# Kernel optimization log

Hardware: AMD Instinct MI355X
Metric: run time of the kernel (lower is better)

Reference implementation:

```python
import jax, jax.numpy as jnp
import numpy as np

L, B, T, N, C, H, K, M = 2, 4, 8, 2048, 2, 64, 3, 32
DIN0, DIN1, DOUT = C + H, 2 * H, 4 * H


def setup_inputs() -> dict:
    key = jax.random.key(0)
    ks = jax.random.split(key, 24)
    s = 0.05
    p = lambda k, shape: jax.random.normal(k, shape, jnp.float32) * s
    return {
        # support matrices, roughly row-normalized random graph
        "G": jax.random.uniform(ks[0], (K, N, N), jnp.float32) * (2.0 / N),
        "x_seq": jax.random.normal(ks[1], (B, T, N, C), jnp.float32),
        "init_h": jnp.zeros((L, B, N, H), jnp.float32),
        "init_c": jnp.zeros((L, B, N, H), jnp.float32),
        "x_meta": jax.random.normal(ks[2], (B, T, M), jnp.float32),
        # layer 0 meta-learner params (dim_in = C+H)
        "lw1_0": p(ks[3], (M, 64)), "lb1_0": p(ks[4], (64,)),
        "lw2_0": p(ks[5], (64, K * DIN0 * DOUT)), "lb2_0": p(ks[6], (K * DIN0 * DOUT,)),
        "bw1_0": p(ks[7], (M, 64)), "bb1_0": p(ks[8], (64,)),
        "bw2_0": p(ks[9], (64, DOUT)), "bb2_0": p(ks[10], (DOUT,)),
        # layer 1 meta-learner params (dim_in = 2H)
        "lw1_1": p(ks[11], (M, 64)), "lb1_1": p(ks[12], (64,)),
        "lw2_1": p(ks[13], (64, K * DIN1 * DOUT)), "lb2_1": p(ks[14], (K * DIN1 * DOUT,)),
        "bw1_1": p(ks[15], (M, 64)), "bb1_1": p(ks[16], (64,)),
        "bw2_1": p(ks[17], (64, DOUT)), "bb2_1": p(ks[18], (DOUT,)),
    }


def _meta_gcn(G, x, meta, lw1, lb1, lw2, lb2, bw1, bb1, bw2, bb2):
    # x: [B, N, din] -> out: [B, N, 4H]
    Bb, Nn, din = x.shape
    # K-hop supports, concatenated along feature dim (k-major, matches torch.cat)
    sup = jnp.einsum('kij,bjd->bikd', G, x).reshape(Bb, Nn, K * din)
    W = (jax.nn.relu(meta @ lw1 + lb1) @ lw2 + lb2).reshape(Bb, K * din, DOUT)
    b = (jax.nn.relu(meta @ bw1 + bb1) @ bw2 + bb2)[:, None, :]
    return jnp.einsum('bnd,bdo->bno', sup, W) + b


def _run_layer(G, xs_t, meta_t, h0, c0, params):
    # xs_t: [T, B, N, din_x], meta_t: [T, B, M]
    def step(carry, inp):
        h, c = carry
        x_t, m_t = inp
        conv = _meta_gcn(G, jnp.concatenate([x_t, h], axis=-1), m_t, *params)
        gi, gf, go, gg = jnp.split(conv, 4, axis=-1)
        c_t = jax.nn.sigmoid(gf) * c + jax.nn.sigmoid(gi) * jnp.tanh(gg)
        h_t = jax.nn.sigmoid(go) * jnp.tanh(c_t)
        return (h_t, c_t), h_t
    (hT, cT), hs = jax.lax.scan(step, (h0, c0), (xs_t, meta_t))
    return hT, cT, hs


def reference(G, x_seq, init_h, init_c, x_meta,
              lw1_0, lb1_0, lw2_0, lb2_0, bw1_0, bb1_0, bw2_0, bb2_0,
              lw1_1, lb1_1, lw2_1, lb2_1, bw1_1, bb1_1, bw2_1, bb2_1):
    xs = jnp.transpose(x_seq, (1, 0, 2, 3))      # [T, B, N, C]
    ms = jnp.transpose(x_meta, (1, 0, 2))        # [T, B, M]
    p0 = (lw1_0, lb1_0, lw2_0, lb2_0, bw1_0, bb1_0, bw2_0, bb2_0)
    p1 = (lw1_1, lb1_1, lw2_1, lb2_1, bw1_1, bb1_1, bw2_1, bb2_1)
    h0T, c0T, hs0 = _run_layer(G, xs, ms, init_h[0], init_c[0], p0)
    h1T, c1T, _ = _run_layer(G, hs0, ms, init_h[1], init_c[1], p1)
    # [2, L, B, N, H]: [final h per layer; final c per layer]
    return jnp.stack([jnp.stack([h0T, h1T]), jnp.stack([c0T, c1T])])
```

## Files before the change

### kernel.cpp

```cpp
#include <hip/hip_runtime.h>
#include <hip/hip_bf16.h>
#include <cstdint>


typedef __hip_bfloat16 bf16;
typedef __attribute__((ext_vector_type(8))) short bf16x8;
typedef __attribute__((ext_vector_type(4))) short s16x4;
typedef __attribute__((ext_vector_type(4)))  float f32x4;
typedef __attribute__((ext_vector_type(16))) float f32x16;
typedef __attribute__((ext_vector_type(4)))  int   i32x4;
typedef __attribute__((ext_vector_type(16))) int   i32x16;
typedef __attribute__((ext_vector_type(2)))  long  l64x2;

__device__ __forceinline__ short f2bf(float f) {
    unsigned u = __builtin_bit_cast(unsigned, f);
    return (short)((u + 0x7fffu + ((u >> 16) & 1u)) >> 16);
}

#define GLD_LDS(gaddr, laddr)                                                  \
    __builtin_amdgcn_global_load_lds(                                          \
        (const __attribute__((address_space(1))) void*)(gaddr),                \
        (__attribute__((address_space(3))) void*)(laddr), 16, 0, 0)

#define OFF_GSW    0u
#define OFF_GI8    25165824u
#define OFF_HFA0   37748736u
#define OFF_HFA1   38273024u
#define OFF_HFB0   38797312u
#define OFF_HFB1   39321600u
#define OFF_XS0T   39845888u
#define OFF_HS0F   40370176u
#define OFF_S0X    48758784u
#define OFF_W0SW   74711040u
#define OFF_W1SW   79429632u
#define OFF_BIAS0  85721088u
#define OFF_BIAS1  85753856u
#define OFF_C0     85786624u
#define OFF_C1     87883776u
#define WS_NEEDED  89980928u

__global__ __launch_bounds__(256) void prep_kernel(
    const float* __restrict__ G, const float* __restrict__ x_seq,
    const float* __restrict__ init_h, const float* __restrict__ init_c,
    bf16* __restrict__ Gsw, l64x2* __restrict__ Gi8,
    l64x2* __restrict__ hfA0, l64x2* __restrict__ hfA1,
    bf16* __restrict__ Xs0T, float* __restrict__ c0, float* __restrict__ c1)
{
    const int T_GSB = 1572864;
    const int T_GI8 = 786432;
    const int T_HF  = 65536;
    const int T_XS  = 262144;
    const int T_C   = 1048576;
    const int TOTAL = T_GSB + T_GI8 + T_HF + T_XS + T_C;
    int stride = gridDim.x * 256;
    for (int idx = blockIdx.x*256 + threadIdx.x; idx < TOTAL; idx += stride) {
        int i0 = idx;
        if (i0 < T_GSB) {
            int lane = i0 & 63, jc = (i0 >> 6) & 127, it32 = (i0 >> 13) & 63, k = i0 >> 19;
            int row = it32*32 + (lane & 31);
            int col = jc*16 + (lane >> 5)*8;
            const float* gp = G + ((size_t)(k*2048 + row))*2048 + col;
            f32x4 v0 = *(const f32x4*)gp, v1 = *(const f32x4*)(gp + 4);
            bf16x8 o;
            #pragma unroll
            for (int e = 0; e < 4; e++) { o[e] = f2bf(v0[e]); o[e+4] = f2bf(v1[e]); }
            *(bf16x8*)((short*)Gsw + (size_t)i0*8) = o;
            continue;
        }
        i0 -= T_GSB;
        if (i0 < T_GI8) {
            int lane = i0 & 63, jcp = (i0 >> 6) & 63, it = (i0 >> 12) & 63, k = i0 >> 18;
            int row = it*32 + (lane & 31);
            l64x2 pr;
            #pragma unroll
            for (int jh = 0; jh < 2; jh++) {
                int col = (2*jcp + jh)*16 + (lane >> 5)*8;
                const float* gp = G + ((size_t)(k*2048 + row))*2048 + col;
                f32x4 v0 = *(const f32x4*)gp, v1 = *(const f32x4*)(gp + 4);
                long r = 0;
                #pragma unroll
                for (int e = 0; e < 4; e++) {
                    int q0 = __float2int_rn(v0[e] * 130048.0f);
                    int q1 = __float2int_rn(v1[e] * 130048.0f);
                    q0 = q0 < 0 ? 0 : (q0 > 127 ? 127 : q0);
                    q1 = q1 < 0 ? 0 : (q1 > 127 ? 127 : q1);
                    r |= ((long)(unsigned char)(char)q0) << (8*e);
                    r |= ((long)(unsigned char)(char)q1) << (8*(e+4));
                }
                pr[jh] = r;
            }
            Gi8[i0] = pr;
            continue;
        }
        i0 -= T_GI8;
        if (i0 < T_HF) {
            int lane = i0 & 63, dc = (i0 >> 6) & 1, jcp = (i0 >> 7) & 63;
            int b = (i0 >> 13) & 3, L = i0 >> 15;
            int d = dc*32 + (lane & 31);
            l64x2 pr;
            #pragma unroll
            for (int jh = 0; jh < 2; jh++) {
                int j0 = (2*jcp + jh)*16 + (lane >> 5)*8;
                long r = 0;
                #pragma unroll
                for (int e = 0; e < 8; e++) {
                    float hv = init_h[((size_t)(L*4 + b)*2048 + j0 + e)*64 + d];
                    int q = __float2int_rn(hv * 127.0f);
                    q = q < -127 ? -127 : (q > 127 ? 127 : q);
                    r |= ((long)(unsigned char)(char)q) << (8*e);
                }
                pr[jh] = r;
            }
            l64x2* dst = (L == 0) ? hfA0 : hfA1;
            dst[i0 & 32767] = pr;
            continue;
        }
        i0 -= T_HF;
        if (i0 < T_XS) {
            int n = i0 >> 11, j = i0 & 2047;
            float v = 0.f;
            if (n < 64) {
                int t = n >> 3, rm = n & 7, b = rm >> 1, cc = rm & 1;
                v = x_seq[(((size_t)b*8 + t)*2048 + j)*2 + cc];
            }
            Xs0T[i0] = __float2bfloat16(v);
            continue;
        }
        i0 -= T_XS;
        if (i0 < 524288) { c0[i0] = init_c[i0]; continue; }
        i0 -= 524288;
        c1[i0] = init_c[524288 + i0];
    }
}

__global__ __launch_bounds__(256) void metaw_kernel(
    const float* __restrict__ x_meta,
    const float* __restrict__ lw1_0, const float* __restrict__ lb1_0,
    const float* __restrict__ lw2_0, const float* __restrict__ lb2_0,
    const float* __restrict__ bw1_0, const float* __restrict__ bb1_0,
    const float* __restrict__ bw2_0, const float* __restrict__ bb2_0,
    const float* __restrict__ lw1_1, const float* __restrict__ lb1_1,
    const float* __restrict__ lw2_1, const float* __restrict__ lb2_1,
    const float* __restrict__ bw1_1, const float* __restrict__ bb1_1,
    const float* __restrict__ bw2_1, const float* __restrict__ bb2_1,
    bf16* __restrict__ W0sw, bf16* __restrict__ W1sw,
    float* __restrict__ bias0, float* __restrict__ bias1)
{
    int tid = threadIdx.x, bid = blockIdx.x;
    const float *w1, *b1v, *w2, *b2v;
    int task, r = 0;
    if (bid < 384)      { task = 0; r = bid;       w1=lw1_1; b1v=lb1_1; w2=lw2_1; b2v=lb2_1; }
    else if (bid < 582) { task = 1; r = bid - 384; w1=lw1_0; b1v=lb1_0; w2=lw2_0; b2v=lb2_0; }
    else if (bid == 582){ task = 2;                w1=bw1_0; b1v=bb1_0; w2=bw2_0; b2v=bb2_0; }
    else                { task = 3;                w1=bw1_1; b1v=bb1_1; w2=bw2_1; b2v=bb2_1; }

    __shared__ float hid[32][64];
    for (int idx = tid; idx < 2048; idx += 256) {
        int tb = idx >> 6, h = idx & 63;
        int tt = tb >> 2, b = tb & 3;
        float a = b1v[h];
        #pragma unroll
        for (int m = 0; m < 32; m++)
            a += x_meta[((size_t)b*8 + tt)*32 + m] * w1[m*64 + h];
        hid[tb][h] = fmaxf(a, 0.f);
    }
    __syncthreads();

    int o = tid;
    int RO = (task == 0) ? 98304 : (task == 1) ? 50688 : 256;
    int ro = (task >= 2) ? o : (r*256 + o);
    float col[64];
    #pragma unroll
    for (int h = 0; h < 64; h++) col[h] = w2[(size_t)h*RO + ro];
    float base = b2v[ro];

    for (int tb = 0; tb < 32; tb++) {
        float v = base;
        #pragma unroll
        for (int h = 0; h < 64; h++) v += hid[tb][h]*col[h];
        if (task == 0) {
            int rp = r, rc = rp >> 5, rr = rp & 31;
            int oc = o >> 4, l = ((rr >> 3) << 4) + (o & 15), e = rr & 7;
            W1sw[(((size_t)tb*12 + rc)*16 + oc)*512 + l*8 + e] = __float2bfloat16(v);
        } else if (task == 1) {
            int k = r/66, d = r - k*66;
            int rp = k*96 + (d < 2 ? 64 + d : d - 2);
            int rc = rp >> 5, rr = rp & 31;
            int oc = o >> 4, l = ((rr >> 3) << 4) + (o & 15), e = rr & 7;
            W0sw[(((size_t)tb*9 + rc)*16 + oc)*512 + l*8 + e] = __float2bfloat16(v);
        } else if (task == 2) bias0[tb*256 + o] = v;
        else                  bias1[tb*256 + o] = v;
    }
}

__global__ __launch_bounds__(256) void s0x_kernel(
    const short* __restrict__ Gsw, const short* __restrict__ Bm,
    bf16* __restrict__ dstB)
{
    __shared__ short lB[128 * 64];
    int bid = blockIdx.x;
    int mt = (bid & 7) * 6 + (bid >> 3);
    int kk = mt >> 4;

    int tid = threadIdx.x, lane = tid & 63, w = tid >> 6;
    int wr = w >> 1, wc = w & 1;
    int l31 = lane & 31, lhi = lane >> 5;

    int rloc = lane >> 3;
    int gsrc = ((lane & 7) ^ rloc) * 8;
    const short* Bb = Bm + gsrc;

    f32x16 acc[2][2];
    #pragma unroll
    for (int a2 = 0; a2 < 2; a2++)
        #pragma unroll
        for (int b2 = 0; b2 < 2; b2++)
            #pragma unroll
            for (int q = 0; q < 16; q++) acc[a2][b2][q] = 0.f;

    for (int kb = 0; kb < 2048; kb += 64) {
        #pragma unroll
        for (int q = 0; q < 4; q++) {
            int row = (w * 4 + q) * 8 + rloc;
            GLD_LDS(Bb + (size_t)row * 2048 + kb, &lB[(w * 4 + q) * 512]);
        }
        __syncthreads();
        #pragma unroll
        for (int ks = 0; ks < 4; ks++) {
            int jc = (kb >> 4) + ks;
            bf16x8 af[2], bf2[2];
            #pragma unroll
            for (int a2 = 0; a2 < 2; a2++) {
                int it32 = (mt & 15) * 4 + wr * 2 + a2;
                af[a2] = *(const bf16x8*)(Gsw +
                    ((((size_t)(kk * 64 + it32)) * 128 + jc) * 64 + lane) * 8);
            }
            #pragma unroll
            for (int b2 = 0; b2 < 2; b2++) {
                int r = wc * 64 + b2 * 32 + l31;
                int cb = (ks * 32 + lhi * 16) ^ ((r & 7) << 4);
                bf2[b2] = *(const bf16x8*)((const char*)lB + r * 128 + cb);
            }
            #pragma unroll
            for (int a2 = 0; a2 < 2; a2++)
                #pragma unroll
                for (int b2 = 0; b2 < 2; b2++)
                    acc[a2][b2] = __builtin_amdgcn_mfma_f32_32x32x16_bf16(
                        af[a2], bf2[b2], acc[a2][b2], 0, 0, 0);
        }
        __syncthreads();
    }

    #pragma unroll
    for (int a2 = 0; a2 < 2; a2++) {
        #pragma unroll
        for (int b2 = 0; b2 < 2; b2++) {
            int gn = wc * 64 + b2 * 32 + l31;
            if (gn >= 64) continue;
            #pragma unroll
            for (int reg = 0; reg < 16; reg++) {
                int gm = (mt & 15) * 128 + wr * 64 + a2 * 32
                         + (reg & 3) + 8 * (reg >> 2) + 4 * lhi;
                dstB[((size_t)kk * 2048 + gm) * 64 + gn] =
                    __float2bfloat16(acc[a2][b2][reg]);
            }
        }
    }
}

#define LD(P, JP)                                                              \
    do { _Pragma("unroll") for (int k = 0; k < 3; k++)                         \
            P##a[k] = Gi8[(((size_t)(k * 64 + it)) * 64 + (JP)) * 64 + lane];  \
         _Pragma("unroll") for (int dc = 0; dc < 2; dc++)                      \
            P##b[dc] = Bfr[(((size_t)(b * 64 + (JP))) * 2 + dc) * 64 + lane];  \
    } while (0)

#define CP(P)                                                                  \
    do { _Pragma("unroll") for (int k = 0; k < 3; k++)                         \
         _Pragma("unroll") for (int dc = 0; dc < 2; dc++) {                    \
            acc6[k * 2 + dc] = __builtin_amdgcn_mfma_i32_32x32x16_i8(          \
                P##a[k][0], P##b[dc][0], acc6[k * 2 + dc], 0, 0, 0);           \
            acc6[k * 2 + dc] = __builtin_amdgcn_mfma_i32_32x32x16_i8(          \
                P##a[k][1], P##b[dc][1], acc6[k * 2 + dc], 0, 0, 0); } }       \
    while (0)

__device__ __forceinline__ void i8_pass(
    i32x16* acc6, const l64x2* __restrict__ Gi8, const l64x2* __restrict__ Bfr,
    int it, int b, int lane, int w)
{
    #pragma unroll
    for (int f = 0; f < 6; f++)
        #pragma unroll
        for (int r = 0; r < 16; r++) acc6[f][r] = 0;
    int jp0 = w * 16;
    l64x2 fAa[3], fAb[2], fBa[3], fBb[2], fCa[3], fCb[2], fDa[3], fDb[2];
    LD(fA, jp0 + 0); LD(fB, jp0 + 1); LD(fC, jp0 + 2); LD(fD, jp0 + 3);
    #pragma unroll 1
    for (int j4 = 0; j4 < 3; j4++) {
        CP(fA); LD(fA, jp0 + j4 * 4 + 4);
        CP(fB); LD(fB, jp0 + j4 * 4 + 5);
        CP(fC); LD(fC, jp0 + j4 * 4 + 6);
        CP(fD); LD(fD, jp0 + j4 * 4 + 7);
    }
    CP(fA); CP(fB); CP(fC); CP(fD);
}

__device__ __forceinline__ void reduce_sup(
    char* lds, char* SUP, i32x16* acc6, int w, int lane)
{
    int* RB = (int*)lds;
    int l31 = lane & 31, lhi = lane >> 5;
    if (w >= 2) {
        #pragma unroll
        for (int f = 0; f < 6; f++)
            #pragma unroll
            for (int qq = 0; qq < 4; qq++) {
                i32x4 v;
                #pragma unroll
                for (int r = 0; r < 4; r++) v[r] = acc6[f][qq * 4 + r];
                *(i32x4*)(RB + ((size_t)((w - 2) * 6 + f)) * 1024 + lane * 16 + qq * 4) = v;
            }
    }
    __syncthreads();
    if (w < 2) {
        #pragma unroll
        for (int f = 0; f < 6; f++)
            #pragma unroll
            for (int r = 0; r < 16; r++)
                acc6[f][r] += RB[((size_t)(w * 6 + f)) * 1024 + lane * 16 + r];
    }
    __syncthreads();
    if (w == 1) {
        #pragma unroll
        for (int f = 0; f < 6; f++)
            #pragma unroll
            for (int qq = 0; qq < 4; qq++) {
                i32x4 v;
                #pragma unroll
                for (int r = 0; r < 4; r++) v[r] = acc6[f][qq * 4 + r];
                *(i32x4*)(RB + (size_t)f * 1024 + lane * 16 + qq * 4) = v;
            }
    }
    __syncthreads();
    if (w == 0) {
        const float SCL = 1.0f / 16516096.0f;
        #pragma unroll
        for (int f = 0; f < 6; f++) {
            int k = f >> 1, dc = f & 1;
            #pragma unroll
            for (int reg = 0; reg < 16; reg++) {
                int s = acc6[f][reg] + RB[(size_t)f * 1024 + lane * 16 + reg];
                float sf = (float)s * SCL;
                int i = (reg & 3) + 8 * (reg >> 2) + 4 * lhi;
                int dpos = k * 64 + dc * 32 + l31;
                *(short*)(SUP + i * 512 + ((dpos * 2) ^ ((i & 15) << 4))) = f2bf(sf);
            }
        }
    }
    __syncthreads();
}

template<int LAYER>
__device__ __forceinline__ void step_part(
    char* lds, int idx, int t,
    const l64x2* __restrict__ Gi8, const short* __restrict__ Sstat,
    const l64x2* __restrict__ hs0f, const short* __restrict__ Wsw,
    const float* __restrict__ bias, float* __restrict__ cbuf,
    const l64x2* __restrict__ hfr_in, long* __restrict__ hfr_out,
    long* __restrict__ hs0f_out, float* __restrict__ out)
{
    constexpr int NC = (LAYER == 0) ? 9 : 12;
    char* SUPs = lds + 24576;
    char* SUPr = lds + 49152;
    short* hT = (short*)(lds + 65536);
    char* hTq = lds + 69632;

    int tid = threadIdx.x, lane = tid & 63, w = tid >> 6;
    int q = idx >> 3;
    int it = (idx & 7) * 8 + (q >> 2), b = q & 3;
    int i0 = it * 32;
    int l15 = lane & 15, lg = lane >> 4;

    i32x16 acc6[6];

    if (LAYER == 0) {
        i8_pass(acc6, Gi8, hfr_in, it, b, lane, w);
        reduce_sup(lds, SUPs, acc6, w, lane);
    } else {
        i8_pass(acc6, Gi8, hfr_in, it, b, lane, w);
        reduce_sup(lds, SUPr, acc6, w, lane);
        i8_pass(acc6, Gi8, hs0f, it, b, lane, w);
        reduce_sup(lds, SUPs, acc6, w, lane);
    }

    f32x4 ag[2][4];
    #pragma unroll
    for (int mi = 0; mi < 2; mi++)
        #pragma unroll
        for (int g = 0; g < 4; g++)
            #pragma unroll
            for (int r = 0; r < 4; r++) ag[mi][g][r] = 0.f;

    const short* WswT = Wsw + (size_t)(t * 4 + b) * NC * 16 * 512;

    #pragma unroll
    for (int rc = 0; rc < NC; rc++) {
        bf16x8 a0, a1;
        if (LAYER == 1) {
            int kk = rc >> 2, dq = rc & 3;
            const char* S = (dq < 2) ? SUPs : SUPr;
            int dqe = (dq < 2) ? dq : (dq - 2);
            int dpb = (kk * 64 + dqe * 32 + lg * 8) * 2;
            a0 = *(const bf16x8*)(S + l15 * 512 + (dpb ^ (l15 << 4)));
            a1 = *(const bf16x8*)(S + (l15 + 16) * 512 + (dpb ^ (l15 << 4)));
        } else {
            int kk = rc / 3, dd = rc - kk * 3;
            if (dd < 2) {
                int dpb = (kk * 64 + dd * 32 + lg * 8) * 2;
                a0 = *(const bf16x8*)(SUPs + l15 * 512 + (dpb ^ (l15 << 4)));
                a1 = *(const bf16x8*)(SUPs + (l15 + 16) * 512 + (dpb ^ (l15 << 4)));
            } else {
                #pragma unroll
                for (int e = 0; e < 8; e++) { a0[e] = 0; a1[e] = 0; }
                if (lg == 0) {
                    unsigned v0 = *(const unsigned*)(Sstat + ((size_t)kk * 2048 + i0 + l15) * 64 + t * 8 + b * 2);
                    unsigned v1 = *(const unsigned*)(Sstat + ((size_t)kk * 2048 + i0 + 16 + l15) * 64 + t * 8 + b * 2);
                    a0[0] = (short)(v0 & 0xffff); a0[1] = (short)(v0 >> 16);
                    a1[0] = (short)(v1 & 0xffff); a1[1] = (short)(v1 >> 16);
                }
            }
        }
        #pragma unroll
        for (int g = 0; g < 4; g++) {
            bf16x8 wf = *(const bf16x8*)(WswT + (((size_t)rc * 16 + (g * 4 + w)) * 64 + lane) * 8);
            ag[0][g] = __builtin_amdgcn_mfma_f32_16x16x32_bf16(a0, wf, ag[0][g], 0, 0, 0);
            ag[1][g] = __builtin_amdgcn_mfma_f32_16x16x32_bf16(a1, wf, ag[1][g], 0, 0, 0);
        }
    }

    int hcol = w * 16 + l15;
    float bia[4];
    #pragma unroll
    for (int g = 0; g < 4; g++) bia[g] = bias[(t * 4 + b) * 256 + g * 64 + hcol];

    #pragma unroll
    for (int mi = 0; mi < 2; mi++) {
        #pragma unroll
        for (int r = 0; r < 4; r++) {
            int iloc = mi * 16 + lg * 4 + r;
            int i = i0 + iloc;
            float gi = ag[mi][0][r] + bia[0];
            float gf = ag[mi][1][r] + bia[1];
            float go = ag[mi][2][r] + bia[2];
            float gg = ag[mi][3][r] + bia[3];
            size_t cidx = ((size_t)b * 2048 + i) * 64 + hcol;
            float c_old = cbuf[cidx];
            float si = 1.f / (1.f + __expf(-gi));
            float sf = 1.f / (1.f + __expf(-gf));
            float so = 1.f / (1.f + __expf(-go));
            float cn = sf * c_old + si * tanhf(gg);
            float hn = so * tanhf(cn);
            cbuf[cidx] = cn;
            hT[iloc * 64 + hcol] = f2bf(hn);
            int hq = __float2int_rn(hn * 127.0f);
            hq = hq < -127 ? -127 : (hq > 127 ? 127 : hq);
            hTq[iloc * 64 + hcol] = (char)hq;
            if (t == 7) {
                out[(((size_t)LAYER * 4 + b) * 2048 + i) * 64 + hcol]       = hn;
                out[(((size_t)(2 + LAYER) * 4 + b) * 2048 + i) * 64 + hcol] = cn;
            }
        }
    }
    __syncthreads();

    {
        int jh = tid >> 7, dc = (tid >> 6) & 1, lane6 = tid & 63;
        long r = 0;
        #pragma unroll
        for (int e = 0; e < 8; e++)
            r |= ((long)(unsigned char)hTq[(jh * 16 + (lane6 >> 5) * 8 + e) * 64
                                           + dc * 32 + (lane6 & 31)]) << (8 * e);
        size_t lidx = ((((size_t)(b * 64 + it)) * 2 + dc) * 64 + lane6) * 2 + jh;
        hfr_out[lidx] = r;
        if (LAYER == 0) hs0f_out[lidx] = r;
    }
}

__global__ __launch_bounds__(256) void combo_kernel(
    const l64x2* __restrict__ Gi8, const short* __restrict__ S0x,
    const l64x2* __restrict__ hs0f_c,
    const short* __restrict__ W0sw, const short* __restrict__ W1sw,
    const float* __restrict__ bias0, const float* __restrict__ bias1,
    float* __restrict__ c0, float* __restrict__ c1,
    long* __restrict__ hfA0, long* __restrict__ hfB0,
    long* __restrict__ hfA1, long* __restrict__ hfB1,
    long* __restrict__ hs0f, float* __restrict__ out, int tau)
{
    __shared__ char lds[71680];
    int bid = blockIdx.x;
    if (bid < 256) {
        int t = tau;
        if (t > 7) return;
        const long* hin  = (t & 1) ? hfB0 : hfA0;
        long*       hout = (t & 1) ? hfA0 : hfB0;
        step_part<0>(lds, bid, t, Gi8, S0x, nullptr, W0sw, bias0, c0,
                     (const l64x2*)hin, hout, hs0f + (size_t)t * 65536, out);
    } else {
        int t = tau - 1;
        if (t < 0) return;
        const long* hin  = (t & 1) ? hfB1 : hfA1;
        long*       hout = (t & 1) ? hfA1 : hfB1;
        step_part<1>(lds, bid - 256, t, Gi8, nullptr,
                     hs0f_c + (size_t)t * 32768, W1sw, bias1, c1,
                     (const l64x2*)hin, hout, nullptr, out);
    }
}

extern "C" void kernel_launch(void* const* d_in, const int* in_sizes, int n_in,
                              void* d_out, int out_size, void* d_ws, size_t ws_size,
                              hipStream_t stream)
{
    const float* G      = (const float*)d_in[0];
    const float* x_seq  = (const float*)d_in[1];
    const float* init_h = (const float*)d_in[2];
    const float* init_c = (const float*)d_in[3];
    const float* x_meta = (const float*)d_in[4];
    const float* lw1_0 = (const float*)d_in[5],  *lb1_0 = (const float*)d_in[6];
    const float* lw2_0 = (const float*)d_in[7],  *lb2_0 = (const float*)d_in[8];
    const float* bw1_0 = (const float*)d_in[9],  *bb1_0 = (const float*)d_in[10];
    const float* bw2_0 = (const float*)d_in[11], *bb2_0 = (const float*)d_in[12];
    const float* lw1_1 = (const float*)d_in[13], *lb1_1 = (const float*)d_in[14];
    const float* lw2_1 = (const float*)d_in[15], *lb2_1 = (const float*)d_in[16];
    const float* bw1_1 = (const float*)d_in[17], *bb1_1 = (const float*)d_in[18];
    const float* bw2_1 = (const float*)d_in[19], *bb2_1 = (const float*)d_in[20];

    if (ws_size < WS_NEEDED) return;

    char* ws = (char*)d_ws;
    bf16*  Gsw   = (bf16*) (ws + OFF_GSW);
    l64x2* Gi8   = (l64x2*)(ws + OFF_GI8);
    l64x2* hfA0  = (l64x2*)(ws + OFF_HFA0);
    l64x2* hfA1  = (l64x2*)(ws + OFF_HFA1);
    l64x2* hfB0  = (l64x2*)(ws + OFF_HFB0);
    l64x2* hfB1  = (l64x2*)(ws + OFF_HFB1);
    bf16*  Xs0T  = (bf16*) (ws + OFF_XS0T);
    l64x2* hs0f  = (l64x2*)(ws + OFF_HS0F);
    bf16*  S0x   = (bf16*) (ws + OFF_S0X);
    bf16*  W0sw  = (bf16*) (ws + OFF_W0SW);
    bf16*  W1sw  = (bf16*) (ws + OFF_W1SW);
    float* bias0 = (float*)(ws + OFF_BIAS0);
    float* bias1 = (float*)(ws + OFF_BIAS1);
    float* c0    = (float*)(ws + OFF_C0);
    float* c1    = (float*)(ws + OFF_C1);
    float* out   = (float*)d_out;

    prep_kernel<<<4096, 256, 0, stream>>>(G, x_seq, init_h, init_c,
                                          Gsw, Gi8, hfA0, hfA1, Xs0T, c0, c1);
    metaw_kernel<<<584, 256, 0, stream>>>(x_meta,
        lw1_0, lb1_0, lw2_0, lb2_0, bw1_0, bb1_0, bw2_0, bb2_0,
        lw1_1, lb1_1, lw2_1, lb2_1, bw1_1, bb1_1, bw2_1, bb2_1,
        W0sw, W1sw, bias0, bias1);

    s0x_kernel<<<48, 256, 0, stream>>>((const short*)Gsw, (const short*)Xs0T, S0x);

    for (int tau = 0; tau < 9; tau++)
        combo_kernel<<<512, 256, 0, stream>>>(Gi8, (const short*)S0x, hs0f,
            (const short*)W0sw, (const short*)W1sw, bias0, bias1, c0, c1,
            (long*)hfA0, (long*)hfB0, (long*)hfA1, (long*)hfB1,
            (long*)hs0f, out, tau);
}
```

Measured before the change: 449.2 us.

## Split-K the S0x GEMM across more blocks and fuse G bf16/int8 prep

```diff
diff --git a/kernel.cpp b/kernel.cpp
--- a/kernel.cpp
+++ b/kernel.cpp
@@ -31,6 +31,7 @@
 #define OFF_XS0T   39845888u
 #define OFF_HS0F   40370176u
 #define OFF_S0X    48758784u
+#define OFF_S0XP   52428800u
 #define OFF_W0SW   74711040u
 #define OFF_W1SW   79429632u
 #define OFF_BIAS0  85721088u
@@ -46,40 +47,29 @@
     l64x2* __restrict__ hfA0, l64x2* __restrict__ hfA1,
     bf16* __restrict__ Xs0T, float* __restrict__ c0, float* __restrict__ c1)
 {
-    const int T_GSB = 1572864;
-    const int T_GI8 = 786432;
+    const int T_GP  = 786432;
     const int T_HF  = 65536;
     const int T_XS  = 262144;
     const int T_C   = 1048576;
-    const int TOTAL = T_GSB + T_GI8 + T_HF + T_XS + T_C;
+    const int TOTAL = T_GP + T_HF + T_XS + T_C;
     int stride = gridDim.x * 256;
     for (int idx = blockIdx.x*256 + threadIdx.x; idx < TOTAL; idx += stride) {
         int i0 = idx;
-        if (i0 < T_GSB) {
-            int lane = i0 & 63, jc = (i0 >> 6) & 127, it32 = (i0 >> 13) & 63, k = i0 >> 19;
-            int row = it32*32 + (lane & 31);
-            int col = jc*16 + (lane >> 5)*8;
-            const float* gp = G + ((size_t)(k*2048 + row))*2048 + col;
-            f32x4 v0 = *(const f32x4*)gp, v1 = *(const f32x4*)(gp + 4);
-            bf16x8 o;
-            #pragma unroll
-            for (int e = 0; e < 4; e++) { o[e] = f2bf(v0[e]); o[e+4] = f2bf(v1[e]); }
-            *(bf16x8*)((short*)Gsw + (size_t)i0*8) = o;
-            continue;
-        }
-        i0 -= T_GSB;
-        if (i0 < T_GI8) {
+        if (i0 < T_GP) {
             int lane = i0 & 63, jcp = (i0 >> 6) & 63, it = (i0 >> 12) & 63, k = i0 >> 18;
             int row = it*32 + (lane & 31);
             l64x2 pr;
             #pragma unroll
             for (int jh = 0; jh < 2; jh++) {
-                int col = (2*jcp + jh)*16 + (lane >> 5)*8;
+                int jc = 2*jcp + jh;
+                int col = jc*16 + (lane >> 5)*8;
                 const float* gp = G + ((size_t)(k*2048 + row))*2048 + col;
                 f32x4 v0 = *(const f32x4*)gp, v1 = *(const f32x4*)(gp + 4);
+                bf16x8 o;
                 long r = 0;
                 #pragma unroll
                 for (int e = 0; e < 4; e++) {
+                    o[e] = f2bf(v0[e]); o[e+4] = f2bf(v1[e]);
                     int q0 = __float2int_rn(v0[e] * 130048.0f);
                     int q1 = __float2int_rn(v1[e] * 130048.0f);
                     q0 = q0 < 0 ? 0 : (q0 > 127 ? 127 : q0);
@@ -87,12 +77,14 @@
                     r |= ((long)(unsigned char)(char)q0) << (8*e);
                     r |= ((long)(unsigned char)(char)q1) << (8*(e+4));
                 }
+                *(bf16x8*)((short*)Gsw +
+                    ((((size_t)(k*64 + it))*128 + jc)*64 + lane)*8) = o;
                 pr[jh] = r;
             }
             Gi8[i0] = pr;
             continue;
         }
-        i0 -= T_GI8;
+        i0 -= T_GP;
         if (i0 < T_HF) {
             int lane = i0 & 63, dc = (i0 >> 6) & 1, jcp = (i0 >> 7) & 63;
             int b = (i0 >> 13) & 3, L = i0 >> 15;
@@ -195,11 +187,13 @@
 
 __global__ __launch_bounds__(256) void s0x_kernel(
     const short* __restrict__ Gsw, const short* __restrict__ Bm,
-    bf16* __restrict__ dstB)
+    float* __restrict__ S0Xp)
 {
     __shared__ short lB[128 * 64];
     int bid = blockIdx.x;
-    int mt = (bid & 7) * 6 + (bid >> 3);
+    int xcd = bid & 7, local = bid >> 3;
+    int mt = xcd * 6 + (local % 6);
+    int sk = local / 6;
     int kk = mt >> 4;
 
     int tid = threadIdx.x, lane = tid & 63, w = tid >> 6;
@@ -218,7 +212,7 @@
             #pragma unroll
             for (int q = 0; q < 16; q++) acc[a2][b2][q] = 0.f;
 
-    for (int kb = 0; kb < 2048; kb += 64) {
+    for (int kb = sk * 512; kb < sk * 512 + 512; kb += 64) {
         #pragma unroll
         for (int q = 0; q < 4; q++) {
             int row = (w * 4 + q) * 8 + rloc;
@@ -261,11 +255,27 @@
             for (int reg = 0; reg < 16; reg++) {
                 int gm = (mt & 15) * 128 + wr * 64 + a2 * 32
                          + (reg & 3) + 8 * (reg >> 2) + 4 * lhi;
-                dstB[((size_t)kk * 2048 + gm) * 64 + gn] =
-                    __float2bfloat16(acc[a2][b2][reg]);
-            }
-        }
-    }
+                S0Xp[(((size_t)sk * 3 + kk) * 2048 + gm) * 64 + gn] = acc[a2][b2][reg];
+            }
+        }
+    }
+}
+
+__global__ __launch_bounds__(256) void s0x_reduce(
+    const float* __restrict__ S0Xp, bf16* __restrict__ S0x)
+{
+    int idx = blockIdx.x * 256 + threadIdx.x;
+    size_t e0 = (size_t)idx * 4;
+    f32x4 s = *(const f32x4*)(S0Xp + e0);
+    #pragma unroll
+    for (int p = 1; p < 4; p++) {
+        f32x4 v = *(const f32x4*)(S0Xp + (size_t)p * 393216 + e0);
+        s[0] += v[0]; s[1] += v[1]; s[2] += v[2]; s[3] += v[3];
+    }
+    s16x4 o;
+    #pragma unroll
+    for (int u = 0; u < 4; u++) o[u] = f2bf(s[u]);
+    *(s16x4*)((short*)S0x + e0) = o;
 }
 
 #define LD(P, JP)                                                              \
@@ -546,6 +556,7 @@
     bf16*  Xs0T  = (bf16*) (ws + OFF_XS0T);
     l64x2* hs0f  = (l64x2*)(ws + OFF_HS0F);
     bf16*  S0x   = (bf16*) (ws + OFF_S0X);
+    float* S0Xp  = (float*)(ws + OFF_S0XP);
     bf16*  W0sw  = (bf16*) (ws + OFF_W0SW);
     bf16*  W1sw  = (bf16*) (ws + OFF_W1SW);
     float* bias0 = (float*)(ws + OFF_BIAS0);
@@ -561,7 +572,8 @@
         lw1_1, lb1_1, lw2_1, lb2_1, bw1_1, bb1_1, bw2_1, bb2_1,
         W0sw, W1sw, bias0, bias1);
 
-    s0x_kernel<<<48, 256, 0, stream>>>((const short*)Gsw, (const short*)Xs0T, S0x);
+    s0x_kernel<<<192, 256, 0, stream>>>((const short*)Gsw, (const short*)Xs0T, S0Xp);
+    s0x_reduce<<<384, 256, 0, stream>>>(S0Xp, S0x);
 
     for (int tau = 0; tau < 9; tau++)
         combo_kernel<<<512, 256, 0, stream>>>(Gi8, (const short*)S0x, hs0f,
```

Result: faster. 411.4 us (-8.4%).
